# Optimization experiments

Hardware: AMD Instinct MI355X
Metric: run time of the kernel (lower is better)

## Reference

```python
import jax, jax.numpy as jnp
import numpy as np

B, N, M, F, K = 32, 256, 64, 128, 64
N_INTERACT_RES, N_ATOM_RES = 3, 2


def ssp(x):
    # shifted softplus, PhysNet activation
    return jax.nn.softplus(x) - jnp.log(2.0).astype(x.dtype)


def res_block(h, W1, b1, W2, b2):
    # PhysNet residual layer: h + W2 @ ssp(W1 @ ssp(h) + b1) + b2
    t = ssp(h)
    t = ssp(t @ W1.T + b1)
    return h + t @ W2.T + b2


def setup_inputs() -> dict:
    key = jax.random.key(0)
    ks = jax.random.split(key, 20)
    sF = 1.0 / np.sqrt(F)
    sK = 1.0 / np.sqrt(K)
    return {
        "x": jax.random.normal(ks[0], (B, N, F), jnp.float32),
        "rbf": jax.random.uniform(ks[1], (B, N, M, K), jnp.float32),
        "neighbor": jax.random.randint(ks[2], (B, N, M), 0, N, jnp.int32),
        "k2f_W": jax.random.normal(ks[3], (F, K), jnp.float32) * sK,  # no bias
        "Wi": jax.random.normal(ks[4], (F, F), jnp.float32) * sF,
        "bi": jnp.zeros((F,), jnp.float32),
        "ires_W1": jax.random.normal(ks[5], (N_INTERACT_RES, F, F), jnp.float32) * sF,
        "ires_b1": jnp.zeros((N_INTERACT_RES, F), jnp.float32),
        "ires_W2": jax.random.normal(ks[6], (N_INTERACT_RES, F, F), jnp.float32) * sF,
        "ires_b2": jnp.zeros((N_INTERACT_RES, F), jnp.float32),
        "Wint": jax.random.normal(ks[7], (F, F), jnp.float32) * sF,
        "bint": jnp.zeros((F,), jnp.float32),
        "u_gate": jnp.ones((F,), jnp.float32),
        "ares_W1": jax.random.normal(ks[8], (N_ATOM_RES, F, F), jnp.float32) * sF,
        "ares_b1": jnp.zeros((N_ATOM_RES, F), jnp.float32),
        "ares_W2": jax.random.normal(ks[9], (N_ATOM_RES, F, F), jnp.float32) * sF,
        "ares_b2": jnp.zeros((N_ATOM_RES, F), jnp.float32),
    }


def reference(x, rbf, neighbor, k2f_W, Wi, bi, ires_W1, ires_b1, ires_W2, ires_b2,
              Wint, bint, u_gate, ares_W1, ares_b1, ares_W2, ares_b2):
    b, n, f = x.shape
    m = neighbor.shape[2]
    xa = ssp(x)                                            # (B,N,F)
    g = jnp.einsum('bnmk,fk->bnmf', rbf, k2f_W)            # RBF filter (B,N,M,F)
    xi = ssp(xa @ Wi.T + bi)                               # self message
    # gather neighbor features: xj[b,n,m,:] = xa[b, neighbor[b,n,m], :]
    idx = jnp.broadcast_to(neighbor.reshape(b, n * m)[:, :, None], (b, n * m, f))
    xj = jnp.take_along_axis(xa, idx, axis=1).reshape(b, n, m, f)
    xj = jnp.sum(xj * g, axis=2)                           # aggregate over neighbors
    v = xi + xj
    for l in range(ires_W1.shape[0]):
        v = res_block(v, ires_W1[l], ires_b1[l], ires_W2[l], ires_b2[l])
    v = ssp(v)
    out = u_gate * x + (v @ Wint.T + bint)
    for l in range(ares_W1.shape[0]):
        out = res_block(out, ares_W1[l], ares_b1[l], ares_W2[l], ares_b2[l])
    return out
```

## Files before the change

kernel.cpp:

```cpp
#include <hip/hip_runtime.h>
#include <math.h>

#define PB 32
#define PN 256
#define PM 64
#define PF 128
#define PK 64
#define ROWS (PB*PN)
#define NTOT (ROWS*PF)

#define OFF_K2F  0
#define OFF_WI   8192
#define OFF_IW1  24576
#define OFF_IW2  73728
#define OFF_WINT 122880
#define OFF_AW1  139264
#define OFF_AW2  172032
#define TOTAL_W  204800

#define XPITCH 136

typedef __attribute__((ext_vector_type(4))) float  floatx4;
typedef __attribute__((ext_vector_type(8))) short  shortx8;

__device__ __forceinline__ unsigned short f2b(float f){
    union { float f; unsigned int i; } c; c.f = f;
    unsigned int x = c.i;
    return (unsigned short)((x + 0x7fffu + ((x >> 16) & 1u)) >> 16);
}
__device__ __forceinline__ float bf2f(unsigned short u){
    union { unsigned int i; float f; } c; c.i = ((unsigned int)u) << 16; return c.f;
}
__device__ __forceinline__ float sspf(float x){
    return fmaxf(x, 0.0f) + log1pf(expf(-fabsf(x))) - 0.69314718055994531f;
}
__device__ __forceinline__ shortx8 pack8(float4 a, float4 b){
    shortx8 r;
    r[0]=(short)f2b(a.x); r[1]=(short)f2b(a.y); r[2]=(short)f2b(a.z); r[3]=(short)f2b(a.w);
    r[4]=(short)f2b(b.x); r[5]=(short)f2b(b.y); r[6]=(short)f2b(b.z); r[7]=(short)f2b(b.w);
    return r;
}

__global__ __launch_bounds__(256) void k_pre(const float* __restrict__ x,
                                             const float* __restrict__ k2f,
                                             const float* __restrict__ Wi,
                                             const float* __restrict__ iW1,
                                             const float* __restrict__ iW2,
                                             const float* __restrict__ Wint,
                                             const float* __restrict__ aW1,
                                             const float* __restrict__ aW2,
                                             float* __restrict__ xa_f,
                                             unsigned short* __restrict__ xa_b,
                                             unsigned short* __restrict__ Wb){
    int i = blockIdx.x * 256 + threadIdx.x;
    if (i < NTOT){
        float v = sspf(x[i]);
        xa_f[i] = v;
        xa_b[i] = f2b(v);
        return;
    }
    int j = i - NTOT;
    if (j >= TOTAL_W) return;
    float v;
    if      (j < OFF_WI)   v = k2f[j - OFF_K2F];
    else if (j < OFF_IW1)  v = Wi[j - OFF_WI];
    else if (j < OFF_IW2)  v = iW1[j - OFF_IW1];
    else if (j < OFF_WINT) v = iW2[j - OFF_IW2];
    else if (j < OFF_AW1)  v = Wint[j - OFF_WINT];
    else if (j < OFF_AW2)  v = aW1[j - OFF_AW1];
    else                   v = aW2[j - OFF_AW2];
    Wb[j] = f2b(v);
}

__global__ __launch_bounds__(256) void k_msg(const float* __restrict__ rbf,
                                             const int* __restrict__ nbr,
                                             const unsigned short* __restrict__ Wk2f,
                                             const float* __restrict__ xa_f,
                                             float* __restrict__ xj){
    const int tid  = threadIdx.x;
    const int bid  = blockIdx.x * 4 + (tid >> 6);
    const int b    = bid >> 8;
    const int lane = tid & 63;
    const int quad = lane >> 4;
    const int l16  = lane & 15;

    const int nbv = nbr[bid*PM + lane];
    const float* xab = xa_f + (size_t)b * PN * PF;

    float s[8];
    #pragma unroll
    for (int ft = 0; ft < 8; ++ft) s[ft] = 0.f;

    const float* rbase = rbf + (size_t)bid * (PM*PK);

    #pragma unroll
    for (int t = 0; t < 4; ++t){
        const float* rrow = rbase + (size_t)(t*16 + l16) * PK;
        shortx8 afrag0 = pack8(*(const float4*)(rrow + quad*8),
                               *(const float4*)(rrow + quad*8 + 4));
        shortx8 afrag1 = pack8(*(const float4*)(rrow + 32 + quad*8),
                               *(const float4*)(rrow + 32 + quad*8 + 4));

        const int mb = t*16 + quad*4;
        int idx0 = __shfl(nbv, mb + 0, 64);
        int idx1 = __shfl(nbv, mb + 1, 64);
        int idx2 = __shfl(nbv, mb + 2, 64);
        int idx3 = __shfl(nbv, mb + 3, 64);

        #pragma unroll
        for (int ft = 0; ft < 8; ++ft){
            const unsigned short* wrow = Wk2f + (size_t)(ft*16 + l16) * PK;
            shortx8 b0 = *(const shortx8*)(wrow +  0 + quad*8);
            shortx8 b1 = *(const shortx8*)(wrow + 32 + quad*8);
            floatx4 acc = {0.f, 0.f, 0.f, 0.f};
            acc = __builtin_amdgcn_mfma_f32_16x16x32_bf16(afrag0, b0, acc, 0, 0, 0);
            acc = __builtin_amdgcn_mfma_f32_16x16x32_bf16(afrag1, b1, acc, 0, 0, 0);
            const int col = ft*16 + l16;
            s[ft] += acc[0] * xab[(size_t)idx0*PF + col];
            s[ft] += acc[1] * xab[(size_t)idx1*PF + col];
            s[ft] += acc[2] * xab[(size_t)idx2*PF + col];
            s[ft] += acc[3] * xab[(size_t)idx3*PF + col];
        }
    }

    #pragma unroll
    for (int ft = 0; ft < 8; ++ft){
        float v = s[ft];
        v += __shfl_xor(v, 16, 64);
        v += __shfl_xor(v, 32, 64);
        if (quad == 0) xj[(size_t)bid*PF + ft*16 + l16] = v;
    }
}

__device__ __forceinline__ void gemm2(const unsigned short* __restrict__ W,
                                      int l16, int quad, int ftbase,
                                      const shortx8 a[4], floatx4 acc[2]){
    #pragma unroll
    for (int f = 0; f < 2; ++f){
        const unsigned short* wrow = W + (size_t)((ftbase+f)*16 + l16) * PF;
        floatx4 c = {0.f, 0.f, 0.f, 0.f};
        #pragma unroll
        for (int ks = 0; ks < 4; ++ks){
            shortx8 bf = *(const shortx8*)(wrow + ks*32 + quad*8);
            c = __builtin_amdgcn_mfma_f32_16x16x32_bf16(a[ks], bf, c, 0, 0, 0);
        }
        acc[f] = c;
    }
}

__device__ __forceinline__ void relayout(unsigned short* Tls,
                                         const unsigned short t16[8],
                                         int l16, int quad, int ftbase,
                                         shortx8 a[4]){
    #pragma unroll
    for (int f = 0; f < 2; ++f)
        #pragma unroll
        for (int r = 0; r < 4; ++r)
            Tls[(quad*4 + r)*XPITCH + (ftbase+f)*16 + l16] = t16[f*4 + r];
    __syncthreads();
    #pragma unroll
    for (int ks = 0; ks < 4; ++ks)
        a[ks] = *(const shortx8*)(Tls + l16*XPITCH + ks*32 + quad*8);
}

__global__ __launch_bounds__(256) void k_chain(const unsigned short* __restrict__ xa_b,
                                               const float* __restrict__ xj,
                                               const float* __restrict__ x,
                                               const unsigned short* __restrict__ Wb,
                                               const float* __restrict__ bi,
                                               const float* __restrict__ ib1,
                                               const float* __restrict__ ib2,
                                               const float* __restrict__ bint,
                                               const float* __restrict__ ugate,
                                               const float* __restrict__ ab1,
                                               const float* __restrict__ ab2,
                                               float* __restrict__ out){
    const int tid  = threadIdx.x;
    const int wave = tid >> 6;
    const int lane = tid & 63;
    const int quad = lane >> 4;
    const int l16  = lane & 15;
    const int ftb  = wave*2;
    const int row0 = blockIdx.x * 16;

    __shared__ unsigned short Tls[2][16 * XPITCH];
    int p = 0;

    int col[2];
    #pragma unroll
    for (int f = 0; f < 2; ++f) col[f] = (ftb+f)*16 + l16;

    const unsigned short* inrow = xa_b + (size_t)(row0 + l16) * PF;
    shortx8 a[4];
    #pragma unroll
    for (int ks = 0; ks < 4; ++ks)
        a[ks] = *(const shortx8*)(inrow + ks*32 + quad*8);

    floatx4 acc[2];
    float V[8];
    unsigned short t16[8];

    gemm2(Wb + OFF_WI, l16, quad, ftb, a, acc);
    #pragma unroll
    for (int f = 0; f < 2; ++f)
        #pragma unroll
        for (int r = 0; r < 4; ++r){
            size_t idx = (size_t)(row0 + quad*4 + r)*PF + col[f];
            float of = sspf(acc[f][r] + bi[col[f]]) + xj[idx];
            V[f*4+r] = of;
            t16[f*4+r] = f2b(sspf(of));
        }
    relayout(Tls[p], t16, l16, quad, ftb, a); p ^= 1;

    for (int l = 0; l < 3; ++l){
        gemm2(Wb + OFF_IW1 + l*PF*PF, l16, quad, ftb, a, acc);
        #pragma unroll
        for (int f = 0; f < 2; ++f)
            #pragma unroll
            for (int r = 0; r < 4; ++r)
                t16[f*4+r] = f2b(sspf(acc[f][r] + ib1[l*PF + col[f]]));
        relayout(Tls[p], t16, l16, quad, ftb, a); p ^= 1;

        gemm2(Wb + OFF_IW2 + l*PF*PF, l16, quad, ftb, a, acc);
        #pragma unroll
        for (int f = 0; f < 2; ++f)
            #pragma unroll
            for (int r = 0; r < 4; ++r){
                V[f*4+r] += acc[f][r] + ib2[l*PF + col[f]];
                t16[f*4+r] = f2b(sspf(V[f*4+r]));
            }
        relayout(Tls[p], t16, l16, quad, ftb, a); p ^= 1;
    }

    gemm2(Wb + OFF_WINT, l16, quad, ftb, a, acc);
    #pragma unroll
    for (int f = 0; f < 2; ++f)
        #pragma unroll
        for (int r = 0; r < 4; ++r){
            size_t idx = (size_t)(row0 + quad*4 + r)*PF + col[f];
            float o = ugate[col[f]] * x[idx] + acc[f][r] + bint[col[f]];
            V[f*4+r] = o;
            t16[f*4+r] = f2b(sspf(o));
        }
    relayout(Tls[p], t16, l16, quad, ftb, a); p ^= 1;

    #pragma unroll
    for (int l = 0; l < 2; ++l){
        gemm2(Wb + OFF_AW1 + l*PF*PF, l16, quad, ftb, a, acc);
        #pragma unroll
        for (int f = 0; f < 2; ++f)
            #pragma unroll
            for (int r = 0; r < 4; ++r)
                t16[f*4+r] = f2b(sspf(acc[f][r] + ab1[l*PF + col[f]]));
        relayout(Tls[p], t16, l16, quad, ftb, a); p ^= 1;

        gemm2(Wb + OFF_AW2 + l*PF*PF, l16, quad, ftb, a, acc);
        if (l == 0){
            #pragma unroll
            for (int f = 0; f < 2; ++f)
                #pragma unroll
                for (int r = 0; r < 4; ++r){
                    V[f*4+r] += acc[f][r] + ab2[l*PF + col[f]];
                    t16[f*4+r] = f2b(sspf(V[f*4+r]));
                }
            relayout(Tls[p], t16, l16, quad, ftb, a); p ^= 1;
        } else {
            #pragma unroll
            for (int f = 0; f < 2; ++f)
                #pragma unroll
                for (int r = 0; r < 4; ++r){
                    size_t idx = (size_t)(row0 + quad*4 + r)*PF + col[f];
                    out[idx] = V[f*4+r] + acc[f][r] + ab2[l*PF + col[f]];
                }
        }
    }
}

extern "C" void kernel_launch(void* const* d_in, const int* in_sizes, int n_in,
                              void* d_out, int out_size, void* d_ws, size_t ws_size,
                              hipStream_t stream){
    const float* x     = (const float*)d_in[0];
    const float* rbf   = (const float*)d_in[1];
    const int*   nbr   = (const int*)d_in[2];
    const float* k2fW  = (const float*)d_in[3];
    const float* Wi    = (const float*)d_in[4];
    const float* bi    = (const float*)d_in[5];
    const float* iW1   = (const float*)d_in[6];
    const float* ib1   = (const float*)d_in[7];
    const float* iW2   = (const float*)d_in[8];
    const float* ib2   = (const float*)d_in[9];
    const float* Wint  = (const float*)d_in[10];
    const float* bint  = (const float*)d_in[11];
    const float* ugate = (const float*)d_in[12];
    const float* aW1   = (const float*)d_in[13];
    const float* ab1   = (const float*)d_in[14];
    const float* aW2   = (const float*)d_in[15];
    const float* ab2   = (const float*)d_in[16];

    char* ws = (char*)d_ws;
    unsigned short* xa_b = (unsigned short*)ws;
    float*          xa_f = (float*)(ws + (2ull  << 20));
    float*          xj   = (float*)(ws + (6ull  << 20));
    unsigned short* Wb   = (unsigned short*)(ws + (10ull << 20));

    k_pre<<<(NTOT + TOTAL_W + 255)/256, 256, 0, stream>>>(
        x, k2fW, Wi, iW1, iW2, Wint, aW1, aW2, xa_f, xa_b, Wb);
    k_msg<<<ROWS/4, 256, 0, stream>>>(rbf, nbr, Wb + OFF_K2F, xa_f, xj);
    k_chain<<<ROWS/16, 256, 0, stream>>>(xa_b, xj, x, Wb,
                                         bi, ib1, ib2, bint, ugate, ab1, ab2,
                                         (float*)d_out);
}
```

Measured before the change: 312.2 us.

## Split k_msg neighbor tiles across four waves per atom with LDS reduction

Each block now handles one atom instead of four, and each of its four waves processes a 16-neighbor tile, replacing the serial 4-iteration loop per wave. All rbf and neighbor loads are issued up front, and the per-wave partial sums are combined through shared memory. This exposes more memory-level parallelism on the rbf stream, which dominates k_msg, at the cost of four times as many blocks, a __syncthreads and the LDS reduction.

```diff
diff --git a/kernel.cpp b/kernel.cpp
--- a/kernel.cpp
+++ b/kernel.cpp
@@ -78,49 +78,42 @@
                                              const float* __restrict__ xa_f,
                                              float* __restrict__ xj){
     const int tid  = threadIdx.x;
-    const int bid  = blockIdx.x * 4 + (tid >> 6);
+    const int t    = tid >> 6;
+    const int bid  = blockIdx.x;
     const int b    = bid >> 8;
     const int lane = tid & 63;
     const int quad = lane >> 4;
     const int l16  = lane & 15;
 
-    const int nbv = nbr[bid*PM + lane];
+    __shared__ float red[4][PF];
+
+    const float* rrow = rbf + (size_t)bid * (PM*PK) + (size_t)(t*16 + l16) * PK;
+    float4 r0 = *(const float4*)(rrow + quad*8);
+    float4 r1 = *(const float4*)(rrow + quad*8 + 4);
+    float4 r2 = *(const float4*)(rrow + 32 + quad*8);
+    float4 r3 = *(const float4*)(rrow + 32 + quad*8 + 4);
+    int4 nb = *(const int4*)(nbr + (size_t)bid*PM + t*16 + quad*4);
+
     const float* xab = xa_f + (size_t)b * PN * PF;
 
+    shortx8 afrag0 = pack8(r0, r1);
+    shortx8 afrag1 = pack8(r2, r3);
+
     float s[8];
     #pragma unroll
-    for (int ft = 0; ft < 8; ++ft) s[ft] = 0.f;
-
-    const float* rbase = rbf + (size_t)bid * (PM*PK);
-
-    #pragma unroll
-    for (int t = 0; t < 4; ++t){
-        const float* rrow = rbase + (size_t)(t*16 + l16) * PK;
-        shortx8 afrag0 = pack8(*(const float4*)(rrow + quad*8),
-                               *(const float4*)(rrow + quad*8 + 4));
-        shortx8 afrag1 = pack8(*(const float4*)(rrow + 32 + quad*8),
-                               *(const float4*)(rrow + 32 + quad*8 + 4));
-
-        const int mb = t*16 + quad*4;
-        int idx0 = __shfl(nbv, mb + 0, 64);
-        int idx1 = __shfl(nbv, mb + 1, 64);
-        int idx2 = __shfl(nbv, mb + 2, 64);
-        int idx3 = __shfl(nbv, mb + 3, 64);
-
-        #pragma unroll
-        for (int ft = 0; ft < 8; ++ft){
-            const unsigned short* wrow = Wk2f + (size_t)(ft*16 + l16) * PK;
-            shortx8 b0 = *(const shortx8*)(wrow +  0 + quad*8);
-            shortx8 b1 = *(const shortx8*)(wrow + 32 + quad*8);
-            floatx4 acc = {0.f, 0.f, 0.f, 0.f};
-            acc = __builtin_amdgcn_mfma_f32_16x16x32_bf16(afrag0, b0, acc, 0, 0, 0);
-            acc = __builtin_amdgcn_mfma_f32_16x16x32_bf16(afrag1, b1, acc, 0, 0, 0);
-            const int col = ft*16 + l16;
-            s[ft] += acc[0] * xab[(size_t)idx0*PF + col];
-            s[ft] += acc[1] * xab[(size_t)idx1*PF + col];
-            s[ft] += acc[2] * xab[(size_t)idx2*PF + col];
-            s[ft] += acc[3] * xab[(size_t)idx3*PF + col];
-        }
+    for (int ft = 0; ft < 8; ++ft){
+        const unsigned short* wrow = Wk2f + (size_t)(ft*16 + l16) * PK;
+        shortx8 b0 = *(const shortx8*)(wrow +  0 + quad*8);
+        shortx8 b1 = *(const shortx8*)(wrow + 32 + quad*8);
+        floatx4 acc = {0.f, 0.f, 0.f, 0.f};
+        acc = __builtin_amdgcn_mfma_f32_16x16x32_bf16(afrag0, b0, acc, 0, 0, 0);
+        acc = __builtin_amdgcn_mfma_f32_16x16x32_bf16(afrag1, b1, acc, 0, 0, 0);
+        const int col = ft*16 + l16;
+        float v =  acc[0] * xab[(size_t)nb.x*PF + col];
+        v       += acc[1] * xab[(size_t)nb.y*PF + col];
+        v       += acc[2] * xab[(size_t)nb.z*PF + col];
+        v       += acc[3] * xab[(size_t)nb.w*PF + col];
+        s[ft] = v;
     }
 
     #pragma unroll
@@ -128,7 +121,11 @@
         float v = s[ft];
         v += __shfl_xor(v, 16, 64);
         v += __shfl_xor(v, 32, 64);
-        if (quad == 0) xj[(size_t)bid*PF + ft*16 + l16] = v;
+        if (quad == 0) red[t][ft*16 + l16] = v;
+    }
+    __syncthreads();
+    if (tid < PF){
+        xj[(size_t)bid*PF + tid] = red[0][tid] + red[1][tid] + red[2][tid] + red[3][tid];
     }
 }
 
@@ -305,7 +302,7 @@
 
     k_pre<<<(NTOT + TOTAL_W + 255)/256, 256, 0, stream>>>(
         x, k2fW, Wi, iW1, iW2, Wint, aW1, aW2, xa_f, xa_b, Wb);
-    k_msg<<<ROWS/4, 256, 0, stream>>>(rbf, nbr, Wb + OFF_K2F, xa_f, xj);
+    k_msg<<<ROWS, 256, 0, stream>>>(rbf, nbr, Wb + OFF_K2F, xa_f, xj);
     k_chain<<<ROWS/16, 256, 0, stream>>>(xa_b, xj, x, Wb,
                                          bi, ib1, ib2, bint, ugate, ab1, ab2,
                                          (float*)d_out);
```

After: 322.5 us. +3.3%, slower.
